# Kernel tuning notes

Measured on AMD Instinct MI355X. Metric: run time of the kernel, lower is better.

Reference implementation:

```python
import jax, jax.numpy as jnp
import numpy as np


def setup_inputs() -> dict:
    key = jax.random.key(0)
    k1, k2, k3 = jax.random.split(key, 3)
    shape = (2, 16, 2048, 64)  # (b, num_heads, seq_len, d_k)
    Q = jax.random.normal(k1, shape, dtype=jnp.float32)
    K = jax.random.normal(k2, shape, dtype=jnp.float32)
    V = jax.random.normal(k3, shape, dtype=jnp.float32)
    return {"Q": Q, "K": K, "V": V}


def reference(Q, K, V):
    # Mathematically identical to the blockwise online-softmax loop:
    # causal softmax attention with scale 1/sqrt(d_k), plus logsumexp L.
    d_k = Q.shape[-1]
    seq_len = Q.shape[2]
    scale = 1.0 / np.sqrt(d_k).astype(np.float32)
    # scores: [b, h, q, k]
    S = jnp.einsum("bhqd,bhkd->bhqk", Q, K) * scale
    causal_mask = jnp.tril(jnp.ones((seq_len, seq_len), dtype=bool))  # k_pos <= q_pos
    S = jnp.where(causal_mask, S, -jnp.inf)
    # L_i = m_i + log(l_i) == logsumexp over key dim (every row has >=1 valid key)
    L = jax.nn.logsumexp(S, axis=-1, keepdims=True)  # [b, h, q, 1]
    P = jnp.exp(S - L)  # normalized probabilities (deferred-normalization result)
    O = jnp.einsum("bhqk,bhkd->bhqd", P, V)
    return O, L
```

## Files before the change

kernel.cpp:

```cpp
#include <hip/hip_runtime.h>
#include <hip/hip_bf16.h>

#define S_LEN 2048
#define DH    64
#define NBH   32
#define KSCALE 0.1803368801111f
#define LN2    0.6931471805599453f
#define MB2    4.0f

typedef short v4s __attribute__((ext_vector_type(4)));
typedef short v8s __attribute__((ext_vector_type(8)));
typedef float v4f __attribute__((ext_vector_type(4)));

__device__ __forceinline__ unsigned short f2bf(float f){
  union { float f; unsigned int u; } v; v.f = f;
  return (unsigned short)((v.u + 0x7FFFu + ((v.u >> 16) & 1u)) >> 16);
}

__device__ __forceinline__ void gld16(void* lds, const void* g){
  __builtin_amdgcn_global_load_lds(
      (const __attribute__((address_space(1))) unsigned int*)g,
      (__attribute__((address_space(3))) unsigned int*)lds, 16, 0, 0);
}

__global__ __launch_bounds__(256) void prep(const float* __restrict__ K,
                                            const float* __restrict__ V,
                                            unsigned short* __restrict__ Kf,
                                            unsigned short* __restrict__ Vf){
  __shared__ unsigned short s[64 * 72];
  const int t   = blockIdx.x;
  const int bh  = blockIdx.y;
  const int tid = threadIdx.x;

  const float* Ksrc = K + ((size_t)bh * S_LEN + t * 64) * DH;
  #pragma unroll
  for (int i = 0; i < 4; ++i){
    int f = tid + i * 256;
    float4 v = ((const float4*)Ksrc)[f];
    int row = f >> 4, col = (f & 15) * 4;
    ushort4 o; o.x = f2bf(v.x); o.y = f2bf(v.y); o.z = f2bf(v.z); o.w = f2bf(v.w);
    *(ushort4*)(&s[row * 72 + col]) = o;
  }
  __syncthreads();
  unsigned short* KfT = Kf + ((size_t)bh * 32 + t) * 4096;
  #pragma unroll
  for (int i = 0; i < 2; ++i){
    int item = tid + i * 256;
    int c = item >> 6, l = item & 63;
    int kb = c >> 1, h = c & 1;
    v8s frag = *(const v8s*)(&s[(kb * 16 + (l & 15)) * 72 + h * 32 + (l >> 4) * 8]);
    *(v8s*)(&KfT[c * 512 + l * 8]) = frag;
  }
  __syncthreads();

  const float* Vsrc = V + ((size_t)bh * S_LEN + t * 64) * DH;
  #pragma unroll
  for (int i = 0; i < 4; ++i){
    int f = tid + i * 256;
    float4 v = ((const float4*)Vsrc)[f];
    int k = f >> 4, d = (f & 15) * 4;
    s[(d + 0) * 72 + k] = f2bf(v.x);
    s[(d + 1) * 72 + k] = f2bf(v.y);
    s[(d + 2) * 72 + k] = f2bf(v.z);
    s[(d + 3) * 72 + k] = f2bf(v.w);
  }
  __syncthreads();
  unsigned short* VfT = Vf + ((size_t)bh * 32 + t) * 4096;
  #pragma unroll
  for (int i = 0; i < 2; ++i){
    int item = tid + i * 256;
    int c = item >> 6, l = item & 63;
    int db = c >> 1, kp = c & 1;
    int dd = db * 16 + (l & 15);
    int kk = kp * 32 + (l >> 4) * 4;
    v4s a = *(const v4s*)(&s[dd * 72 + kk]);
    v4s b = *(const v4s*)(&s[dd * 72 + kk + 16]);
    v8s fr; fr[0]=a[0]; fr[1]=a[1]; fr[2]=a[2]; fr[3]=a[3];
            fr[4]=b[0]; fr[5]=b[1]; fr[6]=b[2]; fr[7]=b[3];
    *(v8s*)(&VfT[c * 512 + l * 8]) = fr;
  }
}

__global__ __launch_bounds__(512, 4) void fa_fwd(
    const float* __restrict__ Q,
    const unsigned short* __restrict__ Kf,
    const unsigned short* __restrict__ Vf,
    float* __restrict__ O, float* __restrict__ L)
{
  __shared__ char smem[2][16384];

  const int tid  = threadIdx.x;
  const int w    = tid >> 6;
  const int lane = tid & 63;
  const int lq   = lane & 15;
  const int g    = lane >> 4;
  const int bid  = blockIdx.x;
  const int half = bid >> 8;
  const int idx  = (bid & 255) >> 5;
  const int p    = half ? (15 - idx) : idx;
  const int bh   = bid & 31;
  const int qt   = (w < 4) ? p : 31 - p;
  const int qw0  = qt * 64 + (w & 3) * 16;
  const int M    = 32 - p;

  const unsigned short* KfB = Kf + (size_t)bh * 32 * 4096;
  const unsigned short* VfB = Vf + (size_t)bh * 32 * 4096;
  const int srcOff = w * 512 + lane * 8;

  auto issue = [&](int t, char* buf){
    gld16(buf        + w * 1024, KfB + (size_t)t * 4096 + srcOff);
    gld16(buf + 8192 + w * 1024, VfB + (size_t)t * 4096 + srcOff);
  };

  v8s qf[2];
  {
    const float* qp = Q + (size_t)(bh * S_LEN + qw0 + lq) * DH + g * 8;
    #pragma unroll
    for (int h = 0; h < 2; ++h){
      float4 a = *(const float4*)(qp + h * 32);
      float4 b = *(const float4*)(qp + h * 32 + 4);
      v8s qv;
      qv[0]=(short)f2bf(a.x*KSCALE); qv[1]=(short)f2bf(a.y*KSCALE);
      qv[2]=(short)f2bf(a.z*KSCALE); qv[3]=(short)f2bf(a.w*KSCALE);
      qv[4]=(short)f2bf(b.x*KSCALE); qv[5]=(short)f2bf(b.y*KSCALE);
      qv[6]=(short)f2bf(b.z*KSCALE); qv[7]=(short)f2bf(b.w*KSCALE);
      qf[h] = qv;
    }
  }

  issue(0, smem[0]);

  v4f zero  = {0.f, 0.f, 0.f, 0.f};
  v4f minit = {-MB2, -MB2, -MB2, -MB2};
  v4f acc[4];
  acc[0] = zero; acc[1] = zero; acc[2] = zero; acc[3] = zero;
  float l = 0.f;

  for (int t = 0; t < M; ++t){
    const int tn = (t + 1 < M) ? t + 1 : t;
    issue(tn, smem[(t + 1) & 1]);
    asm volatile("s_waitcnt vmcnt(2)" ::: "memory");
    __builtin_amdgcn_s_barrier();
    __builtin_amdgcn_sched_barrier(0);

    if (t <= qt){
      const char* kbase = smem[t & 1];
      const char* vbase = smem[t & 1] + 8192;

      float p4[4][4];
      __builtin_amdgcn_s_setprio(1);
      #pragma unroll
      for (int kb = 0; kb < 4; ++kb){
        v4f st = minit;
        v8s k0 = *(const v8s*)(kbase + kb * 2048 +        lane * 16);
        v8s k1 = *(const v8s*)(kbase + kb * 2048 + 1024 + lane * 16);
        st = __builtin_amdgcn_mfma_f32_16x16x32_bf16(k0, qf[0], st, 0, 0, 0);
        st = __builtin_amdgcn_mfma_f32_16x16x32_bf16(k1, qf[1], st, 0, 0, 0);
        p4[kb][0] = st[0]; p4[kb][1] = st[1]; p4[kb][2] = st[2]; p4[kb][3] = st[3];
      }
      __builtin_amdgcn_s_setprio(0);

      if (t == qt){
        #pragma unroll
        for (int kb = 0; kb < 4; ++kb){
          #pragma unroll
          for (int r = 0; r < 4; ++r){
            const int krow = t * 64 + kb * 16 + g * 4 + r;
            if (krow > qw0 + lq) p4[kb][r] = -INFINITY;
          }
        }
      }

      #pragma unroll
      for (int kb = 0; kb < 4; ++kb)
        #pragma unroll
        for (int r = 0; r < 4; ++r){
          const float pe = __builtin_amdgcn_exp2f(p4[kb][r]);
          p4[kb][r] = pe;
          l += pe;
        }

      __builtin_amdgcn_s_setprio(1);
      #pragma unroll
      for (int kp = 0; kp < 2; ++kp){
        unsigned u0, u1, u2, u3;
        asm("v_cvt_pk_bf16_f32 %0, %1, %2" : "=v"(u0) : "v"(p4[2*kp  ][0]), "v"(p4[2*kp  ][1]));
        asm("v_cvt_pk_bf16_f32 %0, %1, %2" : "=v"(u1) : "v"(p4[2*kp  ][2]), "v"(p4[2*kp  ][3]));
        asm("v_cvt_pk_bf16_f32 %0, %1, %2" : "=v"(u2) : "v"(p4[2*kp+1][0]), "v"(p4[2*kp+1][1]));
        asm("v_cvt_pk_bf16_f32 %0, %1, %2" : "=v"(u3) : "v"(p4[2*kp+1][2]), "v"(p4[2*kp+1][3]));
        union { unsigned u[2]; v4s s; } P0, P1;
        P0.u[0] = u0; P0.u[1] = u1;
        P1.u[0] = u2; P1.u[1] = u3;
        #pragma unroll
        for (int db = 0; db < 4; ++db){
          v8s vv = *(const v8s*)(vbase + (db * 2 + kp) * 1024 + lane * 16);
          v4s va0 = {vv[0], vv[1], vv[2], vv[3]};
          v4s va1 = {vv[4], vv[5], vv[6], vv[7]};
          acc[db] = __builtin_amdgcn_mfma_f32_16x16x16bf16_1k(va0, P0.s, acc[db], 0, 0, 0);
          acc[db] = __builtin_amdgcn_mfma_f32_16x16x16bf16_1k(va1, P1.s, acc[db], 0, 0, 0);
        }
      }
      __builtin_amdgcn_s_setprio(0);
    }
    __builtin_amdgcn_s_barrier();
    __builtin_amdgcn_sched_barrier(0);
  }

  l += __shfl_xor(l, 16);
  l += __shfl_xor(l, 32);
  const float invl = 1.f / l;
  float* Op = O + ((size_t)bh * S_LEN + qw0 + lq) * DH + g * 4;
  #pragma unroll
  for (int db = 0; db < 4; ++db){
    v4f o = acc[db] * invl;
    *(v4f*)(Op + db * 16) = o;
  }
  if (g == 0)
    L[(size_t)bh * S_LEN + qw0 + lq] = logf(l) + MB2 * LN2;
}

__global__ __launch_bounds__(64) void fa_naive(
    const float* __restrict__ Q, const float* __restrict__ K,
    const float* __restrict__ V, float* __restrict__ O, float* __restrict__ L)
{
  const int q  = blockIdx.x;
  const int bh = blockIdx.y;
  const int d  = threadIdx.x;
  const float qv = Q[(size_t)(bh * S_LEN + q) * DH + d];
  float m = -INFINITY, l = 0.f, o = 0.f;
  for (int k = 0; k <= q; ++k){
    float s = qv * K[(size_t)(bh * S_LEN + k) * DH + d];
    #pragma unroll
    for (int off = 32; off > 0; off >>= 1) s += __shfl_xor(s, off);
    s *= 0.125f;
    const float mn = fmaxf(m, s);
    const float sfc = expf(m - mn);
    const float pe = expf(s - mn);
    l = l * sfc + pe;
    o = o * sfc + pe * V[(size_t)(bh * S_LEN + k) * DH + d];
    m = mn;
  }
  O[(size_t)(bh * S_LEN + q) * DH + d] = o / l;
  if (d == 0) L[(size_t)bh * S_LEN + q] = m + logf(l);
}

extern "C" void kernel_launch(void* const* d_in, const int* in_sizes, int n_in,
                              void* d_out, int out_size, void* d_ws, size_t ws_size,
                              hipStream_t stream)
{
  (void)in_sizes; (void)n_in; (void)out_size;
  const float* Q = (const float*)d_in[0];
  const float* K = (const float*)d_in[1];
  const float* V = (const float*)d_in[2];
  float* O = (float*)d_out;
  float* L = O + (size_t)NBH * S_LEN * DH;

  const size_t half = (size_t)NBH * S_LEN * DH * sizeof(unsigned short);
  if (ws_size >= 2 * half){
    unsigned short* Kf = (unsigned short*)d_ws;
    unsigned short* Vf = Kf + (size_t)NBH * S_LEN * DH;
    prep<<<dim3(S_LEN / 64, NBH), 256, 0, stream>>>(K, V, Kf, Vf);
    fa_fwd<<<dim3(512), 512, 0, stream>>>(Q, Kf, Vf, O, L);
  } else {
    fa_naive<<<dim3(S_LEN, NBH), 64, 0, stream>>>(Q, K, V, O, L);
  }
}
```

Baseline: 42.52 us.

## Split KV tile across waves with cross-wave reduction instead of per-wave query rows

Each block now handles one 64-row query tile with 4 waves, and each wave owns one 16-key slice of every KV tile while computing all four query subtiles. Partial output accumulators and row sums are reduced through shared memory at the end. The old paired-tile load balancing is dropped in favour of 1024 blocks scheduled longest-first. The intent is to cut per-wave LDS reads of K and V and the idle waves on diagonal tiles. In exchange it adds a four-pass LDS reduction epilogue with extra barriers and holds more accumulator registers per wave.

```diff
diff --git a/kernel.cpp b/kernel.cpp
--- a/kernel.cpp
+++ b/kernel.cpp
@@ -81,13 +81,13 @@
   }
 }
 
-__global__ __launch_bounds__(512, 4) void fa_fwd(
+__global__ __launch_bounds__(256, 3) void fa_fwd(
     const float* __restrict__ Q,
     const unsigned short* __restrict__ Kf,
     const unsigned short* __restrict__ Vf,
     float* __restrict__ O, float* __restrict__ L)
 {
-  __shared__ char smem[2][16384];
+  __shared__ __align__(16) char smem[2][16384];
 
   const int tid  = threadIdx.x;
   const int w    = tid >> 6;
@@ -95,26 +95,26 @@
   const int lq   = lane & 15;
   const int g    = lane >> 4;
   const int bid  = blockIdx.x;
-  const int half = bid >> 8;
-  const int idx  = (bid & 255) >> 5;
-  const int p    = half ? (15 - idx) : idx;
+  const int qt   = 31 - (bid >> 5);
   const int bh   = bid & 31;
-  const int qt   = (w < 4) ? p : 31 - p;
-  const int qw0  = qt * 64 + (w & 3) * 16;
-  const int M    = 32 - p;
+  const int M    = qt + 1;
 
   const unsigned short* KfB = Kf + (size_t)bh * 32 * 4096;
   const unsigned short* VfB = Vf + (size_t)bh * 32 * 4096;
-  const int srcOff = w * 512 + lane * 8;
 
   auto issue = [&](int t, char* buf){
-    gld16(buf        + w * 1024, KfB + (size_t)t * 4096 + srcOff);
-    gld16(buf + 8192 + w * 1024, VfB + (size_t)t * 4096 + srcOff);
+    #pragma unroll
+    for (int i = 0; i < 2; ++i){
+      const int slot = tid + i * 256;
+      gld16(buf        + slot * 16, KfB + (size_t)t * 4096 + slot * 8);
+      gld16(buf + 8192 + slot * 16, VfB + (size_t)t * 4096 + slot * 8);
+    }
   };
 
-  v8s qf[2];
-  {
-    const float* qp = Q + (size_t)(bh * S_LEN + qw0 + lq) * DH + g * 8;
+  v8s qf[4][2];
+  #pragma unroll
+  for (int s = 0; s < 4; ++s){
+    const float* qp = Q + (size_t)(bh * S_LEN + qt * 64 + s * 16 + lq) * DH + g * 8;
     #pragma unroll
     for (int h = 0; h < 2; ++h){
       float4 a = *(const float4*)(qp + h * 32);
@@ -124,99 +124,125 @@
       qv[2]=(short)f2bf(a.z*KSCALE); qv[3]=(short)f2bf(a.w*KSCALE);
       qv[4]=(short)f2bf(b.x*KSCALE); qv[5]=(short)f2bf(b.y*KSCALE);
       qv[6]=(short)f2bf(b.z*KSCALE); qv[7]=(short)f2bf(b.w*KSCALE);
-      qf[h] = qv;
+      qf[s][h] = qv;
     }
   }
 
   issue(0, smem[0]);
 
-  v4f zero  = {0.f, 0.f, 0.f, 0.f};
-  v4f minit = {-MB2, -MB2, -MB2, -MB2};
-  v4f acc[4];
-  acc[0] = zero; acc[1] = zero; acc[2] = zero; acc[3] = zero;
-  float l = 0.f;
+  const v4f zero  = {0.f, 0.f, 0.f, 0.f};
+  const v4f minit = {-MB2, -MB2, -MB2, -MB2};
+  v4f acc[4][4];
+  #pragma unroll
+  for (int s = 0; s < 4; ++s)
+    #pragma unroll
+    for (int db = 0; db < 4; ++db) acc[s][db] = zero;
+  float l4[4] = {0.f, 0.f, 0.f, 0.f};
+
+  const int kb    = w;
+  const int koff0 = (kb * 2    ) * 1024 + lane * 16;
+  const int koff1 = (kb * 2 + 1) * 1024 + lane * 16;
+  const int vsub  = (kb >> 1) * 1024 + (kb & 1) * 8 + lane * 16;
 
   for (int t = 0; t < M; ++t){
     const int tn = (t + 1 < M) ? t + 1 : t;
     issue(tn, smem[(t + 1) & 1]);
-    asm volatile("s_waitcnt vmcnt(2)" ::: "memory");
+    asm volatile("s_waitcnt vmcnt(4)" ::: "memory");
     __builtin_amdgcn_s_barrier();
     __builtin_amdgcn_sched_barrier(0);
 
-    if (t <= qt){
-      const char* kbase = smem[t & 1];
-      const char* vbase = smem[t & 1] + 8192;
-
-      float p4[4][4];
-      __builtin_amdgcn_s_setprio(1);
+    const char* kbase = smem[t & 1];
+    const char* vbase = smem[t & 1] + 8192;
+
+    v8s kf0 = *(const v8s*)(kbase + koff0);
+    v8s kf1 = *(const v8s*)(kbase + koff1);
+    v4s vv[4];
+    #pragma unroll
+    for (int db = 0; db < 4; ++db)
+      vv[db] = *(const v4s*)(vbase + db * 2048 + vsub);
+
+    float p4[4][4];
+    __builtin_amdgcn_s_setprio(1);
+    #pragma unroll
+    for (int s = 0; s < 4; ++s){
+      v4f st = minit;
+      st = __builtin_amdgcn_mfma_f32_16x16x32_bf16(kf0, qf[s][0], st, 0, 0, 0);
+      st = __builtin_amdgcn_mfma_f32_16x16x32_bf16(kf1, qf[s][1], st, 0, 0, 0);
+      p4[s][0] = st[0]; p4[s][1] = st[1]; p4[s][2] = st[2]; p4[s][3] = st[3];
+    }
+    __builtin_amdgcn_s_setprio(0);
+
+    if (t == qt){
       #pragma unroll
-      for (int kb = 0; kb < 4; ++kb){
-        v4f st = minit;
-        v8s k0 = *(const v8s*)(kbase + kb * 2048 +        lane * 16);
-        v8s k1 = *(const v8s*)(kbase + kb * 2048 + 1024 + lane * 16);
-        st = __builtin_amdgcn_mfma_f32_16x16x32_bf16(k0, qf[0], st, 0, 0, 0);
-        st = __builtin_amdgcn_mfma_f32_16x16x32_bf16(k1, qf[1], st, 0, 0, 0);
-        p4[kb][0] = st[0]; p4[kb][1] = st[1]; p4[kb][2] = st[2]; p4[kb][3] = st[3];
+      for (int s = 0; s < 4; ++s)
+        #pragma unroll
+        for (int r = 0; r < 4; ++r)
+          if (kb * 16 + g * 4 + r > s * 16 + lq) p4[s][r] = -INFINITY;
+    }
+
+    v4s pf[4];
+    #pragma unroll
+    for (int s = 0; s < 4; ++s){
+      #pragma unroll
+      for (int r = 0; r < 4; ++r){
+        const float pe = __builtin_amdgcn_exp2f(p4[s][r]);
+        p4[s][r] = pe;
+        l4[s] += pe;
       }
-      __builtin_amdgcn_s_setprio(0);
-
-      if (t == qt){
-        #pragma unroll
-        for (int kb = 0; kb < 4; ++kb){
-          #pragma unroll
-          for (int r = 0; r < 4; ++r){
-            const int krow = t * 64 + kb * 16 + g * 4 + r;
-            if (krow > qw0 + lq) p4[kb][r] = -INFINITY;
-          }
-        }
-      }
-
-      #pragma unroll
-      for (int kb = 0; kb < 4; ++kb)
-        #pragma unroll
-        for (int r = 0; r < 4; ++r){
-          const float pe = __builtin_amdgcn_exp2f(p4[kb][r]);
-          p4[kb][r] = pe;
-          l += pe;
-        }
-
-      __builtin_amdgcn_s_setprio(1);
-      #pragma unroll
-      for (int kp = 0; kp < 2; ++kp){
-        unsigned u0, u1, u2, u3;
-        asm("v_cvt_pk_bf16_f32 %0, %1, %2" : "=v"(u0) : "v"(p4[2*kp  ][0]), "v"(p4[2*kp  ][1]));
-        asm("v_cvt_pk_bf16_f32 %0, %1, %2" : "=v"(u1) : "v"(p4[2*kp  ][2]), "v"(p4[2*kp  ][3]));
-        asm("v_cvt_pk_bf16_f32 %0, %1, %2" : "=v"(u2) : "v"(p4[2*kp+1][0]), "v"(p4[2*kp+1][1]));
-        asm("v_cvt_pk_bf16_f32 %0, %1, %2" : "=v"(u3) : "v"(p4[2*kp+1][2]), "v"(p4[2*kp+1][3]));
-        union { unsigned u[2]; v4s s; } P0, P1;
-        P0.u[0] = u0; P0.u[1] = u1;
-        P1.u[0] = u2; P1.u[1] = u3;
-        #pragma unroll
-        for (int db = 0; db < 4; ++db){
-          v8s vv = *(const v8s*)(vbase + (db * 2 + kp) * 1024 + lane * 16);
-          v4s va0 = {vv[0], vv[1], vv[2], vv[3]};
-          v4s va1 = {vv[4], vv[5], vv[6], vv[7]};
-          acc[db] = __builtin_amdgcn_mfma_f32_16x16x16bf16_1k(va0, P0.s, acc[db], 0, 0, 0);
-          acc[db] = __builtin_amdgcn_mfma_f32_16x16x16bf16_1k(va1, P1.s, acc[db], 0, 0, 0);
-        }
-      }
-      __builtin_amdgcn_s_setprio(0);
-    }
+      unsigned u0, u1;
+      asm("v_cvt_pk_bf16_f32 %0, %1, %2" : "=v"(u0) : "v"(p4[s][0]), "v"(p4[s][1]));
+      asm("v_cvt_pk_bf16_f32 %0, %1, %2" : "=v"(u1) : "v"(p4[s][2]), "v"(p4[s][3]));
+      union { unsigned u[2]; v4s s4; } P; P.u[0] = u0; P.u[1] = u1;
+      pf[s] = P.s4;
+    }
+
+    __builtin_amdgcn_s_setprio(1);
+    #pragma unroll
+    for (int s = 0; s < 4; ++s){
+      acc[s][0] = __builtin_amdgcn_mfma_f32_16x16x16bf16_1k(vv[0], pf[s], acc[s][0], 0, 0, 0);
+      acc[s][1] = __builtin_amdgcn_mfma_f32_16x16x16bf16_1k(vv[1], pf[s], acc[s][1], 0, 0, 0);
+      acc[s][2] = __builtin_amdgcn_mfma_f32_16x16x16bf16_1k(vv[2], pf[s], acc[s][2], 0, 0, 0);
+      acc[s][3] = __builtin_amdgcn_mfma_f32_16x16x16bf16_1k(vv[3], pf[s], acc[s][3], 0, 0, 0);
+    }
+    __builtin_amdgcn_s_setprio(0);
     __builtin_amdgcn_s_barrier();
     __builtin_amdgcn_sched_barrier(0);
   }
 
-  l += __shfl_xor(l, 16);
-  l += __shfl_xor(l, 32);
-  const float invl = 1.f / l;
-  float* Op = O + ((size_t)bh * S_LEN + qw0 + lq) * DH + g * 4;
+  asm volatile("s_waitcnt vmcnt(0)" ::: "memory");
+  __builtin_amdgcn_sched_barrier(0);
+  __syncthreads();
+
+  #pragma unroll
+  for (int s = 0; s < 4; ++s){
+    l4[s] += __shfl_xor(l4[s], 16);
+    l4[s] += __shfl_xor(l4[s], 32);
+  }
+  float* Lr = (float*)smem[1];
+  if (lane < 16){
+    #pragma unroll
+    for (int s = 0; s < 4; ++s) Lr[(w * 4 + s) * 16 + lane] = l4[s];
+  }
+  __syncthreads();
+  const float lfw = Lr[(0 * 4 + w) * 16 + lq] + Lr[(1 * 4 + w) * 16 + lq]
+                  + Lr[(2 * 4 + w) * 16 + lq] + Lr[(3 * 4 + w) * 16 + lq];
+  const float invw = 1.f / lfw;
+
+  v4f* Or = (v4f*)smem[0];
+  float* Ob = O + ((size_t)bh * S_LEN + qt * 64 + w * 16 + lq) * DH;
   #pragma unroll
   for (int db = 0; db < 4; ++db){
-    v4f o = acc[db] * invl;
-    *(v4f*)(Op + db * 16) = o;
-  }
-  if (g == 0)
-    L[(size_t)bh * S_LEN + qw0 + lq] = logf(l) + MB2 * LN2;
+    __syncthreads();
+    #pragma unroll
+    for (int s = 0; s < 4; ++s) Or[((w * 4 + s) * 16 + lq) * 4 + g] = acc[s][db];
+    __syncthreads();
+    v4f o = Or[((0 * 4 + w) * 16 + lq) * 4 + g] + Or[((1 * 4 + w) * 16 + lq) * 4 + g]
+          + Or[((2 * 4 + w) * 16 + lq) * 4 + g] + Or[((3 * 4 + w) * 16 + lq) * 4 + g];
+    o *= invw;
+    *(v4f*)(Ob + db * 16 + g * 4) = o;
+  }
+  if (lane < 16)
+    L[(size_t)bh * S_LEN + qt * 64 + w * 16 + lane] = logf(lfw) + MB2 * LN2;
 }
 
 __global__ __launch_bounds__(64) void fa_naive(
@@ -260,7 +286,7 @@
     unsigned short* Kf = (unsigned short*)d_ws;
     unsigned short* Vf = Kf + (size_t)NBH * S_LEN * DH;
     prep<<<dim3(S_LEN / 64, NBH), 256, 0, stream>>>(K, V, Kf, Vf);
-    fa_fwd<<<dim3(512), 512, 0, stream>>>(Q, Kf, Vf, O, L);
+    fa_fwd<<<dim3(1024), 256, 0, stream>>>(Q, Kf, Vf, O, L);
   } else {
     fa_naive<<<dim3(S_LEN, NBH), 64, 0, stream>>>(Q, K, V, O, L);
   }
```

Result: slower. 48.82 us (+14.8%).
